# Kernel tuning notes

Hardware: AMD Instinct MI355X
Metric: run time of the kernel (lower is better)

## Reference

```python
import jax, jax.numpy as jnp
import numpy as np

N_NODES = 50000
N_EDGES = 800000
IN_DIM = 128
HID_DIM = 128
NUM_GRAPHS = 64


def gcn_conv(x, edge_index, W, b):
    """PyG GCNConv: symmetric-normalized aggregation with self-loops.
    out = D^{-1/2} (A + I) D^{-1/2} (x @ W) + b
    """
    n = x.shape[0]
    loop = jnp.arange(n, dtype=edge_index.dtype)
    src = jnp.concatenate([edge_index[0], loop])  # [E+N]
    dst = jnp.concatenate([edge_index[1], loop])
    deg = jax.ops.segment_sum(jnp.ones_like(dst, x.dtype), dst, num_segments=n)
    dinv = jnp.where(deg > 0, jax.lax.rsqrt(deg), 0.0)
    norm = dinv[src] * dinv[dst]  # [E+N]
    h = x @ W  # [N, H] transform before propagate (PyG order)
    msg = h[src] * norm[:, None]  # [E+N, H] gathered+scaled messages
    out = jax.ops.segment_sum(msg, dst, num_segments=n)  # scatter-add
    return out + b


def global_mean_pool(x, batch, num_graphs):
    s = jax.ops.segment_sum(x, batch, num_segments=num_graphs)
    cnt = jax.ops.segment_sum(jnp.ones((x.shape[0],), x.dtype), batch, num_segments=num_graphs)
    return s / jnp.maximum(cnt, 1.0)[:, None]


def setup_inputs() -> dict:
    key = jax.random.key(0)
    ks = jax.random.split(key, 8)
    x = jax.random.normal(ks[0], (N_NODES, IN_DIM), dtype=jnp.float32)
    edge_index = jax.random.randint(ks[1], (2, N_EDGES), 0, N_NODES, dtype=jnp.int64)
    batch = jnp.sort(jax.random.randint(ks[2], (N_NODES,), 0, NUM_GRAPHS, dtype=jnp.int64))
    s1 = 1.0 / np.sqrt(IN_DIM)
    s2 = 1.0 / np.sqrt(HID_DIM)
    W1 = jax.random.uniform(ks[3], (IN_DIM, HID_DIM), jnp.float32, -s1, s1)
    b1 = jnp.zeros((HID_DIM,), jnp.float32)
    W2 = jax.random.uniform(ks[4], (HID_DIM, HID_DIM), jnp.float32, -s2, s2)
    b2 = jnp.zeros((HID_DIM,), jnp.float32)
    Wc = jax.random.uniform(ks[5], (HID_DIM, 1), jnp.float32, -s2, s2)
    bc = jnp.zeros((1,), jnp.float32)
    return {"x": x, "edge_index": edge_index, "batch": batch,
            "W1": W1, "b1": b1, "W2": W2, "b2": b2, "Wc": Wc, "bc": bc}


def reference(x, edge_index, batch, W1, b1, W2, b2, Wc, bc):
    h = jax.nn.relu(gcn_conv(x, edge_index, W1, b1))
    # dropout p=0.1 is identity in eval mode
    h = gcn_conv(h, edge_index, W2, b2)
    g = global_mean_pool(h, batch, NUM_GRAPHS)  # [G, H]
    return jax.nn.sigmoid(g @ Wc + bc)  # [G, 1]
```

## Files before the change

### kernel.cpp

```cpp
#include <hip/hip_runtime.h>
#include <hip/hip_bf16.h>
#include <hip/hip_fp16.h>

#define N_NODES 50000
#define N_EDGES 800000
#define DIM     128
#define NG      64
#define GN      16
#define CAP     48
#define AGG_EB  256
#define LAXP    136

#define NBIN    196
#define SORT_B  250
#define EPB     3200

#define CAST_B  1563
#define VB_B    129
#define WF_B    8

typedef float  f2_t  __attribute__((ext_vector_type(2)));
typedef float  f32x4 __attribute__((ext_vector_type(4)));
typedef _Float16 f16x8 __attribute__((ext_vector_type(8)));
typedef _Float16 f16x4 __attribute__((ext_vector_type(4)));

__global__ void k_prep(const int* __restrict__ ei, int* __restrict__ binCnt,
                       const float4* __restrict__ x4, uint4* __restrict__ xq4,
                       const float* __restrict__ W2, const float* __restrict__ Wc,
                       const float* __restrict__ b2, float* __restrict__ v,
                       float* __restrict__ beta2,
                       const float* __restrict__ W1, f16x8* __restrict__ w1f) {
    __shared__ float red[4];
    __shared__ int hist[256];
    int bid = blockIdx.x, t = threadIdx.x;
    if (bid < SORT_B) {
        hist[t] = 0;
        __syncthreads();
        int base = bid * EPB;
        for (int r = 0; r < 13; r++) {
            int idx = r * 256 + t;
            if (idx < EPB) {
                int d = ei[N_EDGES + base + idx];
                atomicAdd(&hist[d >> 8], 1);
            }
        }
        __syncthreads();
        if (t < NBIN && hist[t] > 0) atomicAdd(&binCnt[t], hist[t]);
    } else if (bid < SORT_B + CAST_B) {
        int idx = (bid - SORT_B) * 256 + t;
        if (idx < N_NODES * DIM / 16) {
            uint4 o;
            unsigned* op = (unsigned*)&o;
            #pragma unroll
            for (int q = 0; q < 4; q++) {
                float4 f = x4[idx * 4 + q];
                int p = 0;
                p = __builtin_amdgcn_cvt_pk_fp8_f32(f.x, f.y, p, false);
                p = __builtin_amdgcn_cvt_pk_fp8_f32(f.z, f.w, p, true);
                op[q] = (unsigned)p;
            }
            xq4[idx] = o;
        }
    } else if (bid < SORT_B + CAST_B + VB_B) {
        int b = bid - (SORT_B + CAST_B);
        float p = 0.f;
        if (t < DIM) p = (b < DIM) ? W2[b * DIM + t] * Wc[t] : b2[t] * Wc[t];
        #pragma unroll
        for (int off = 32; off > 0; off >>= 1) p += __shfl_down(p, off, 64);
        if ((t & 63) == 0) red[t >> 6] = p;
        __syncthreads();
        if (t == 0) {
            float s = red[0] + red[1];
            if (b < DIM) v[b] = s; else beta2[0] = s;
        }
    } else {
        int idx = (bid - (SORT_B + CAST_B + VB_B)) * 256 + t;
        int ntile = idx >> 8, kb = (idx >> 6) & 3, l = idx & 63;
        int kbase = kb * 32 + (l >> 4) * 8;
        int n = ntile * 16 + (l & 15);
        f16x8 o;
        #pragma unroll
        for (int j = 0; j < 8; j++) o[j] = (_Float16)W1[(kbase + j) * DIM + n];
        w1f[idx] = o;
    }
}

__global__ void k_scatter(const int* __restrict__ ei, const int* __restrict__ binCnt,
                          int* __restrict__ binCur, int* __restrict__ binOff,
                          unsigned int* __restrict__ sorted) {
    __shared__ int soff[256];
    __shared__ int hist[256];
    __shared__ int cur[256];
    int bid = blockIdx.x, t = threadIdx.x;
    int c = (t < NBIN) ? binCnt[t] : 0;
    soff[t] = c;
    #pragma unroll
    for (int o = 1; o < 256; o <<= 1) {
        __syncthreads();
        int v2 = (t >= o) ? soff[t - o] : 0;
        __syncthreads();
        soff[t] += v2;
    }
    __syncthreads();
    int excl = soff[t] - c;
    if (bid == 0 && t < NBIN) binOff[t] = excl;
    hist[t] = 0;
    __syncthreads();
    int base = bid * EPB;
    for (int r = 0; r < 13; r++) {
        int idx = r * 256 + t;
        if (idx < EPB) {
            int d = ei[N_EDGES + base + idx];
            atomicAdd(&hist[d >> 8], 1);
        }
    }
    __syncthreads();
    if (t < NBIN && hist[t] > 0) cur[t] = excl + atomicAdd(&binCur[t], hist[t]);
    __syncthreads();
    for (int r = 0; r < 13; r++) {
        int idx = r * 256 + t;
        if (idx < EPB) {
            int e = base + idx;
            int s = ei[e];
            int d = ei[N_EDGES + e];
            int pos = atomicAdd(&cur[d >> 8], 1);
            sorted[pos] = (unsigned)s | ((unsigned)(d & 255) << 16);
        }
    }
}

__global__ void k_deg(const unsigned int* __restrict__ sorted,
                      const int* __restrict__ binOff, int* __restrict__ deg) {
    __shared__ int cnt[256];
    int b = blockIdx.x, t = threadIdx.x;
    cnt[t] = 0;
    __syncthreads();
    int lo = binOff[b];
    int hi = (b == NBIN - 1) ? N_EDGES : binOff[b + 1];
    for (int i = lo + t; i < hi; i += 256)
        atomicAdd(&cnt[sorted[i] >> 16], 1);
    __syncthreads();
    int node = b * 256 + t;
    if (node < N_NODES) deg[node] = cnt[t];
}

__global__ void k_build(const unsigned int* __restrict__ sorted,
                        const int* __restrict__ binOff, const int* __restrict__ deg,
                        unsigned int* __restrict__ csr) {
    __shared__ int cur[256];
    int b = blockIdx.x, t = threadIdx.x;
    cur[t] = 0;
    __syncthreads();
    int lo = binOff[b];
    int hi = (b == NBIN - 1) ? N_EDGES : binOff[b + 1];
    for (int i = lo + t; i < hi; i += 256) {
        unsigned e = sorted[i];
        unsigned src = e & 0xFFFFu;
        unsigned dLow = e >> 16;
        int pos = atomicAdd(&cur[dLow], 1);
        if (pos < CAP) {
            float w = rsqrtf((float)deg[src] + 1.f);
            unsigned hw = (unsigned)__half_as_ushort(__float2half(w));
            csr[(b * 256 + dLow) * CAP + pos] = src | (hw << 16);
        }
    }
}

__global__ __launch_bounds__(512) void k_node(
    const unsigned int* __restrict__ xq,
    const unsigned int* __restrict__ csr,
    const f16x8* __restrict__ w1f,
    const float* __restrict__ b1,
    const float* __restrict__ v, const int* __restrict__ deg,
    float* __restrict__ z2) {
    __shared__ _Float16 laxh[GN * LAXP];
    __shared__ float redm[GN * 8];
    int tid = threadIdx.x;
    int w = tid >> 6, l = tid & 63;
    int half = l >> 5, hl = l & 31;
    int node0 = blockIdx.x * GN;

    {
        int i = node0 + 2 * w + half;
        int len = min(deg[i], CAP);
        float di = rsqrtf((float)deg[i] + 1.f);

        unsigned su = xq[(size_t)i * 32 + hl];
        f2_t s01 = __builtin_amdgcn_cvt_pk_f32_fp8((int)su, false);
        f2_t s23 = __builtin_amdgcn_cvt_pk_f32_fp8((int)su, true);
        float ax[8], ay[8], az[8], aw[8];
        #pragma unroll
        for (int k = 0; k < 8; k++) { ax[k] = 0.f; ay[k] = 0.f; az[k] = 0.f; aw[k] = 0.f; }
        ax[0] = di * s01.x; ay[0] = di * s01.y;
        az[0] = di * s23.x; aw[0] = di * s23.y;

        int lenmax = max(len, __shfl_xor(len, 32, 64));
        int lmp = (lenmax + 7) & ~7;
        const uint4* csr4 = (const uint4*)csr;
        int base4 = i * (CAP / 4);
        for (int j = 0; j < lmp; j += 8) {
            uint4 ca = csr4[base4 + (j >> 2)];
            uint4 cb = csr4[base4 + (j >> 2) + 1];
            unsigned pe[8] = {ca.x, ca.y, ca.z, ca.w, cb.x, cb.y, cb.z, cb.w};
            unsigned q[8];
            #pragma unroll
            for (int k = 0; k < 8; k++)
                q[k] = xq[(size_t)(pe[k] & 0xFFFFu) * 32 + hl];
            float wgt[8];
            #pragma unroll
            for (int k = 0; k < 8; k++)
                wgt[k] = (j + k < len)
                    ? __half2float(__ushort_as_half((unsigned short)(pe[k] >> 16))) : 0.f;
            #pragma unroll
            for (int k = 0; k < 8; k++) {
                f2_t e01 = __builtin_amdgcn_cvt_pk_f32_fp8((int)q[k], false);
                f2_t e23 = __builtin_amdgcn_cvt_pk_f32_fp8((int)q[k], true);
                ax[k] = fmaf(wgt[k], e01.x, ax[k]);
                ay[k] = fmaf(wgt[k], e01.y, ay[k]);
                az[k] = fmaf(wgt[k], e23.x, az[k]);
                aw[k] = fmaf(wgt[k], e23.y, aw[k]);
            }
        }
        float a0 = 0.f, a1 = 0.f, a2 = 0.f, a3 = 0.f;
        #pragma unroll
        for (int k = 0; k < 8; k++) { a0 += ax[k]; a1 += ay[k]; a2 += az[k]; a3 += aw[k]; }
        f16x4 pk;
        pk[0] = (_Float16)(di * a0); pk[1] = (_Float16)(di * a1);
        pk[2] = (_Float16)(di * a2); pk[3] = (_Float16)(di * a3);
        *(f16x4*)&laxh[(2 * w + half) * LAXP + 4 * hl] = pk;
    }
    __syncthreads();

    f32x4 acc = {0.f, 0.f, 0.f, 0.f};
    #pragma unroll
    for (int kb = 0; kb < 4; kb++) {
        f16x8 af = *(const f16x8*)&laxh[(l & 15) * LAXP + kb * 32 + (l >> 4) * 8];
        f16x8 bf = w1f[(w * 4 + kb) * 64 + l];
        acc = __builtin_amdgcn_mfma_f32_16x16x32_f16(af, bf, acc, 0, 0, 0);
    }
    int n = w * 16 + (l & 15);
    float bn = b1[n], vn = v[n];
    #pragma unroll
    for (int r = 0; r < 4; r++) {
        float p = fmaxf(acc[r] + bn, 0.f) * vn;
        p += __shfl_xor(p, 1, 64);
        p += __shfl_xor(p, 2, 64);
        p += __shfl_xor(p, 4, 64);
        p += __shfl_xor(p, 8, 64);
        if ((l & 15) == 0) redm[((l >> 4) * 4 + r) * 8 + w] = p;
    }
    __syncthreads();
    if (tid < GN) {
        float s = 0.f;
        #pragma unroll
        for (int q = 0; q < 8; q++) s += redm[tid * 8 + q];
        z2[node0 + tid] = rsqrtf((float)deg[node0 + tid] + 1.f) * s;
    }
}

__global__ void k_aggz(const float* __restrict__ z2, const int* __restrict__ deg,
                       const int* __restrict__ ei, const int* __restrict__ batch,
                       float* __restrict__ gpartE, float* __restrict__ gpartN,
                       int* __restrict__ gcnt) {
    int bid = blockIdx.x, t = threadIdx.x;
    if (bid < AGG_EB) {
        __shared__ float bs[4][NG];
        bs[t >> 6][t & 63] = 0.f;
        __syncthreads();
        int wg = t >> 6;
        for (int base = bid * 1024; base < N_EDGES; base += AGG_EB * 1024) {
            #pragma unroll
            for (int k = 0; k < 4; k++) {
                int e = base + k * 256 + t;
                if (e < N_EDGES) {
                    int s = ei[e];
                    int d = ei[N_EDGES + e];
                    float dv = rsqrtf((float)deg[d] + 1.f);
                    atomicAdd(&bs[wg][batch[d]], dv * z2[s]);
                }
            }
        }
        __syncthreads();
        if (t < NG) gpartE[bid * NG + t] = bs[0][t] + bs[1][t] + bs[2][t] + bs[3][t];
    } else {
        __shared__ int range[2];
        __shared__ float rs[4];
        int g = bid - AGG_EB;
        if (t < 2) {
            int key = g + t;
            int lo = 0, hi = N_NODES;
            while (lo < hi) { int m = (lo + hi) >> 1; if (batch[m] < key) lo = m + 1; else hi = m; }
            range[t] = lo;
        }
        __syncthreads();
        int lo = range[0], hi = range[1];
        float loc = 0.f;
        for (int i = lo + t; i < hi; i += 256)
            loc += rsqrtf((float)deg[i] + 1.f) * z2[i];
        #pragma unroll
        for (int off = 32; off > 0; off >>= 1) loc += __shfl_down(loc, off, 64);
        if ((t & 63) == 0) rs[t >> 6] = loc;
        __syncthreads();
        if (t == 0) {
            gpartN[g] = rs[0] + rs[1] + rs[2] + rs[3];
            gcnt[g] = hi - lo;
        }
    }
}

__global__ void k_final(const float* __restrict__ gpartE, const float* __restrict__ gpartN,
                        const int* __restrict__ gcnt, const float* __restrict__ beta2,
                        const float* __restrict__ bcin, float* __restrict__ out) {
    __shared__ float acc[4][NG];
    int t = threadIdx.x;
    int g = t & 63, c = t >> 6;
    float s = 0.f;
    for (int k = 0; k < AGG_EB / 4; k++)
        s += gpartE[(c * (AGG_EB / 4) + k) * NG + g];
    acc[c][g] = s;
    __syncthreads();
    if (t < NG) {
        float tot = acc[0][t] + acc[1][t] + acc[2][t] + acc[3][t] + gpartN[t];
        int cnt = gcnt[t];
        float val = tot / (float)(cnt > 0 ? cnt : 1) + beta2[0] + bcin[0];
        out[t] = 1.f / (1.f + expf(-val));
    }
}

extern "C" void kernel_launch(void* const* d_in, const int* in_sizes, int n_in,
                              void* d_out, int out_size, void* d_ws, size_t ws_size,
                              hipStream_t stream) {
    const float* x   = (const float*)d_in[0];
    const int*   ei  = (const int*)  d_in[1];
    const int*   bat = (const int*)  d_in[2];
    const float* W1  = (const float*)d_in[3];
    const float* b1  = (const float*)d_in[4];
    const float* W2  = (const float*)d_in[5];
    const float* b2  = (const float*)d_in[6];
    const float* Wc  = (const float*)d_in[7];
    const float* bc  = (const float*)d_in[8];
    float* out = (float*)d_out;

    char* w = (char*)d_ws;
    size_t off = 0;
    auto alloc = [&](size_t bytes) -> void* {
        void* p = w + off;
        off = (off + bytes + 255) & ~(size_t)255;
        return p;
    };
    int*   binCnt  = (int*)  alloc(NBIN * 4);
    int*   binCur  = (int*)  alloc(NBIN * 4);
    size_t zero_len = off;
    int*   binOff  = (int*)  alloc(NBIN * 4);
    int*   deg     = (int*)  alloc(N_NODES * 4);
    float* z2      = (float*)alloc(N_NODES * 4);
    float* v       = (float*)alloc(DIM * 4);
    float* beta2   = (float*)alloc(4);
    float* gpartE  = (float*)alloc((size_t)AGG_EB * NG * 4);
    float* gpartN  = (float*)alloc(NG * 4);
    int*   gcnt    = (int*)  alloc(NG * 4);
    f16x8* w1f     = (f16x8*)alloc(2048 * 16);
    unsigned int* xq     = (unsigned int*)alloc((size_t)N_NODES * DIM);
    unsigned int* sorted = (unsigned int*)alloc((size_t)N_EDGES * 4);
    unsigned int* csr    = (unsigned int*)alloc((size_t)N_NODES * CAP * 4);
    (void)ws_size; (void)in_sizes; (void)n_in; (void)out_size;

    hipMemsetAsync(d_ws, 0, zero_len, stream);

    dim3 b256(256);
    k_prep<<<dim3(SORT_B + CAST_B + VB_B + WF_B), b256, 0, stream>>>(
        ei, binCnt, (const float4*)x, (uint4*)xq, W2, Wc, b2, v, beta2, W1, w1f);
    k_scatter<<<dim3(SORT_B), b256, 0, stream>>>(ei, binCnt, binCur, binOff, sorted);
    k_deg<<<dim3(NBIN), b256, 0, stream>>>(sorted, binOff, deg);
    k_build<<<dim3(NBIN), b256, 0, stream>>>(sorted, binOff, deg, csr);
    k_node<<<dim3(N_NODES / GN), dim3(512), 0, stream>>>(
        xq, csr, w1f, b1, v, deg, z2);
    k_aggz<<<dim3(AGG_EB + NG), b256, 0, stream>>>(z2, deg, ei, bat, gpartE, gpartN, gcnt);
    k_final<<<dim3(1), b256, 0, stream>>>(gpartE, gpartN, gcnt, beta2, bc, out);
}
```

Baseline: 169.9 us.

## Build CSR with global atomics and prescale features by source degree

Replaces the binned counting sort (histogram, scatter, deg, build kernels) with a single pass that uses global atomicAdd on per-node degree to place 16-bit source ids directly into a fixed-capacity CSR. The source-side normalization is folded into the fp8 feature cast (x scaled by dinv before quantization), so the aggregation loop becomes plain adds with a zero sentinel row for padding. It also packs batch id and fp16 dinv per node for the pooling kernel. This removes three launches and the sorted buffer and halves CSR size, but the neighbor order within each CSR row is now nondeterministic and it relies on heavy global atomic contention.

```diff
diff --git a/kernel.cpp b/kernel.cpp
--- a/kernel.cpp
+++ b/kernel.cpp
@@ -11,10 +11,7 @@
 #define AGG_EB  256
 #define LAXP    136
 
-#define NBIN    196
-#define SORT_B  250
-#define EPB     3200
-
+#define BUILD_B 782
 #define CAST_B  1563
 #define VB_B    129
 #define WF_B    8
@@ -24,45 +21,28 @@
 typedef _Float16 f16x8 __attribute__((ext_vector_type(8)));
 typedef _Float16 f16x4 __attribute__((ext_vector_type(4)));
 
-__global__ void k_prep(const int* __restrict__ ei, int* __restrict__ binCnt,
-                       const float4* __restrict__ x4, uint4* __restrict__ xq4,
+__global__ void k_prep(const int* __restrict__ ei, int* __restrict__ deg,
+                       unsigned short* __restrict__ csr,
                        const float* __restrict__ W2, const float* __restrict__ Wc,
                        const float* __restrict__ b2, float* __restrict__ v,
                        float* __restrict__ beta2,
                        const float* __restrict__ W1, f16x8* __restrict__ w1f) {
     __shared__ float red[4];
-    __shared__ int hist[256];
     int bid = blockIdx.x, t = threadIdx.x;
-    if (bid < SORT_B) {
-        hist[t] = 0;
-        __syncthreads();
-        int base = bid * EPB;
-        for (int r = 0; r < 13; r++) {
-            int idx = r * 256 + t;
-            if (idx < EPB) {
-                int d = ei[N_EDGES + base + idx];
-                atomicAdd(&hist[d >> 8], 1);
-            }
-        }
-        __syncthreads();
-        if (t < NBIN && hist[t] > 0) atomicAdd(&binCnt[t], hist[t]);
-    } else if (bid < SORT_B + CAST_B) {
-        int idx = (bid - SORT_B) * 256 + t;
-        if (idx < N_NODES * DIM / 16) {
-            uint4 o;
-            unsigned* op = (unsigned*)&o;
-            #pragma unroll
-            for (int q = 0; q < 4; q++) {
-                float4 f = x4[idx * 4 + q];
-                int p = 0;
-                p = __builtin_amdgcn_cvt_pk_fp8_f32(f.x, f.y, p, false);
-                p = __builtin_amdgcn_cvt_pk_fp8_f32(f.z, f.w, p, true);
-                op[q] = (unsigned)p;
-            }
-            xq4[idx] = o;
-        }
-    } else if (bid < SORT_B + CAST_B + VB_B) {
-        int b = bid - (SORT_B + CAST_B);
+    if (bid < BUILD_B) {
+        int base = bid * 1024;
+        #pragma unroll
+        for (int k = 0; k < 4; k++) {
+            int e = base + k * 256 + t;
+            if (e < N_EDGES) {
+                int s = ei[e];
+                int d = ei[N_EDGES + e];
+                int pos = atomicAdd(&deg[d], 1);
+                if (pos < CAP) csr[(size_t)d * CAP + pos] = (unsigned short)s;
+            }
+        }
+    } else if (bid < BUILD_B + VB_B) {
+        int b = bid - BUILD_B;
         float p = 0.f;
         if (t < DIM) p = (b < DIM) ? W2[b * DIM + t] * Wc[t] : b2[t] * Wc[t];
         #pragma unroll
@@ -74,7 +54,7 @@
             if (b < DIM) v[b] = s; else beta2[0] = s;
         }
     } else {
-        int idx = (bid - (SORT_B + CAST_B + VB_B)) * 256 + t;
+        int idx = (bid - (BUILD_B + VB_B)) * 256 + t;
         int ntile = idx >> 8, kb = (idx >> 6) & 3, l = idx & 63;
         int kbase = kb * 32 + (l >> 4) * 8;
         int n = ntile * 16 + (l & 15);
@@ -85,90 +65,37 @@
     }
 }
 
-__global__ void k_scatter(const int* __restrict__ ei, const int* __restrict__ binCnt,
-                          int* __restrict__ binCur, int* __restrict__ binOff,
-                          unsigned int* __restrict__ sorted) {
-    __shared__ int soff[256];
-    __shared__ int hist[256];
-    __shared__ int cur[256];
-    int bid = blockIdx.x, t = threadIdx.x;
-    int c = (t < NBIN) ? binCnt[t] : 0;
-    soff[t] = c;
+__global__ void k_cast(const float4* __restrict__ x4, uint4* __restrict__ xq4,
+                       const int* __restrict__ deg, const int* __restrict__ batch,
+                       unsigned int* __restrict__ bd) {
+    int idx = blockIdx.x * 256 + threadIdx.x;
+    if (idx >= (N_NODES + 1) * 8) return;
+    if (idx >= N_NODES * 8) {
+        xq4[idx] = make_uint4(0u, 0u, 0u, 0u);
+        return;
+    }
+    int node = idx >> 3;
+    float di = rsqrtf((float)deg[node] + 1.f);
+    uint4 o;
+    unsigned* op = (unsigned*)&o;
     #pragma unroll
-    for (int o = 1; o < 256; o <<= 1) {
-        __syncthreads();
-        int v2 = (t >= o) ? soff[t - o] : 0;
-        __syncthreads();
-        soff[t] += v2;
-    }
-    __syncthreads();
-    int excl = soff[t] - c;
-    if (bid == 0 && t < NBIN) binOff[t] = excl;
-    hist[t] = 0;
-    __syncthreads();
-    int base = bid * EPB;
-    for (int r = 0; r < 13; r++) {
-        int idx = r * 256 + t;
-        if (idx < EPB) {
-            int d = ei[N_EDGES + base + idx];
-            atomicAdd(&hist[d >> 8], 1);
-        }
-    }
-    __syncthreads();
-    if (t < NBIN && hist[t] > 0) cur[t] = excl + atomicAdd(&binCur[t], hist[t]);
-    __syncthreads();
-    for (int r = 0; r < 13; r++) {
-        int idx = r * 256 + t;
-        if (idx < EPB) {
-            int e = base + idx;
-            int s = ei[e];
-            int d = ei[N_EDGES + e];
-            int pos = atomicAdd(&cur[d >> 8], 1);
-            sorted[pos] = (unsigned)s | ((unsigned)(d & 255) << 16);
-        }
-    }
-}
-
-__global__ void k_deg(const unsigned int* __restrict__ sorted,
-                      const int* __restrict__ binOff, int* __restrict__ deg) {
-    __shared__ int cnt[256];
-    int b = blockIdx.x, t = threadIdx.x;
-    cnt[t] = 0;
-    __syncthreads();
-    int lo = binOff[b];
-    int hi = (b == NBIN - 1) ? N_EDGES : binOff[b + 1];
-    for (int i = lo + t; i < hi; i += 256)
-        atomicAdd(&cnt[sorted[i] >> 16], 1);
-    __syncthreads();
-    int node = b * 256 + t;
-    if (node < N_NODES) deg[node] = cnt[t];
-}
-
-__global__ void k_build(const unsigned int* __restrict__ sorted,
-                        const int* __restrict__ binOff, const int* __restrict__ deg,
-                        unsigned int* __restrict__ csr) {
-    __shared__ int cur[256];
-    int b = blockIdx.x, t = threadIdx.x;
-    cur[t] = 0;
-    __syncthreads();
-    int lo = binOff[b];
-    int hi = (b == NBIN - 1) ? N_EDGES : binOff[b + 1];
-    for (int i = lo + t; i < hi; i += 256) {
-        unsigned e = sorted[i];
-        unsigned src = e & 0xFFFFu;
-        unsigned dLow = e >> 16;
-        int pos = atomicAdd(&cur[dLow], 1);
-        if (pos < CAP) {
-            float w = rsqrtf((float)deg[src] + 1.f);
-            unsigned hw = (unsigned)__half_as_ushort(__float2half(w));
-            csr[(b * 256 + dLow) * CAP + pos] = src | (hw << 16);
-        }
+    for (int q = 0; q < 4; q++) {
+        float4 f = x4[idx * 4 + q];
+        int p = 0;
+        p = __builtin_amdgcn_cvt_pk_fp8_f32(di * f.x, di * f.y, p, false);
+        p = __builtin_amdgcn_cvt_pk_fp8_f32(di * f.z, di * f.w, p, true);
+        op[q] = (unsigned)p;
+    }
+    xq4[idx] = o;
+    if ((idx & 7) == 0) {
+        unsigned hw = (unsigned)__half_as_ushort(__float2half(di));
+        bd[node] = ((unsigned)batch[node] & 0xFFFFu) | (hw << 16);
     }
 }
 
 __global__ __launch_bounds__(512) void k_node(
     const unsigned int* __restrict__ xq,
-    const unsigned int* __restrict__ csr,
+    const unsigned short* __restrict__ csr,
     const f16x8* __restrict__ w1f,
     const float* __restrict__ b1,
     const float* __restrict__ v, const int* __restrict__ deg,
@@ -182,8 +109,9 @@
 
     {
         int i = node0 + 2 * w + half;
-        int len = min(deg[i], CAP);
-        float di = rsqrtf((float)deg[i] + 1.f);
+        int dg = deg[i];
+        int len = min(dg, CAP);
+        float di = rsqrtf((float)dg + 1.f);
 
         unsigned su = xq[(size_t)i * 32 + hl];
         f2_t s01 = __builtin_amdgcn_cvt_pk_f32_fp8((int)su, false);
@@ -191,34 +119,28 @@
         float ax[8], ay[8], az[8], aw[8];
         #pragma unroll
         for (int k = 0; k < 8; k++) { ax[k] = 0.f; ay[k] = 0.f; az[k] = 0.f; aw[k] = 0.f; }
-        ax[0] = di * s01.x; ay[0] = di * s01.y;
-        az[0] = di * s23.x; aw[0] = di * s23.y;
+        ax[0] = s01.x; ay[0] = s01.y;
+        az[0] = s23.x; aw[0] = s23.y;
 
         int lenmax = max(len, __shfl_xor(len, 32, 64));
         int lmp = (lenmax + 7) & ~7;
-        const uint4* csr4 = (const uint4*)csr;
-        int base4 = i * (CAP / 4);
+        const uint4* csr4 = (const uint4*)(csr + (size_t)i * CAP);
         for (int j = 0; j < lmp; j += 8) {
-            uint4 ca = csr4[base4 + (j >> 2)];
-            uint4 cb = csr4[base4 + (j >> 2) + 1];
-            unsigned pe[8] = {ca.x, ca.y, ca.z, ca.w, cb.x, cb.y, cb.z, cb.w};
+            uint4 cw = csr4[j >> 3];
+            unsigned cw8[4] = {cw.x, cw.y, cw.z, cw.w};
             unsigned q[8];
             #pragma unroll
-            for (int k = 0; k < 8; k++)
-                q[k] = xq[(size_t)(pe[k] & 0xFFFFu) * 32 + hl];
-            float wgt[8];
-            #pragma unroll
-            for (int k = 0; k < 8; k++)
-                wgt[k] = (j + k < len)
-                    ? __half2float(__ushort_as_half((unsigned short)(pe[k] >> 16))) : 0.f;
+            for (int k = 0; k < 8; k++) {
+                unsigned id = (cw8[k >> 1] >> ((k & 1) * 16)) & 0xFFFFu;
+                unsigned idc = (j + k < len) ? id : (unsigned)N_NODES;
+                q[k] = xq[(size_t)idc * 32 + hl];
+            }
             #pragma unroll
             for (int k = 0; k < 8; k++) {
                 f2_t e01 = __builtin_amdgcn_cvt_pk_f32_fp8((int)q[k], false);
                 f2_t e23 = __builtin_amdgcn_cvt_pk_f32_fp8((int)q[k], true);
-                ax[k] = fmaf(wgt[k], e01.x, ax[k]);
-                ay[k] = fmaf(wgt[k], e01.y, ay[k]);
-                az[k] = fmaf(wgt[k], e23.x, az[k]);
-                aw[k] = fmaf(wgt[k], e23.y, aw[k]);
+                ax[k] += e01.x; ay[k] += e01.y;
+                az[k] += e23.x; aw[k] += e23.y;
             }
         }
         float a0 = 0.f, a1 = 0.f, a2 = 0.f, a3 = 0.f;
@@ -258,7 +180,7 @@
     }
 }
 
-__global__ void k_aggz(const float* __restrict__ z2, const int* __restrict__ deg,
+__global__ void k_aggz(const float* __restrict__ z2, const unsigned int* __restrict__ bd,
                        const int* __restrict__ ei, const int* __restrict__ batch,
                        float* __restrict__ gpartE, float* __restrict__ gpartN,
                        int* __restrict__ gcnt) {
@@ -275,8 +197,9 @@
                 if (e < N_EDGES) {
                     int s = ei[e];
                     int d = ei[N_EDGES + e];
-                    float dv = rsqrtf((float)deg[d] + 1.f);
-                    atomicAdd(&bs[wg][batch[d]], dv * z2[s]);
+                    unsigned u = bd[d];
+                    float dv = __half2float(__ushort_as_half((unsigned short)(u >> 16)));
+                    atomicAdd(&bs[wg][u & 63u], dv * z2[s]);
                 }
             }
         }
@@ -296,7 +219,7 @@
         int lo = range[0], hi = range[1];
         float loc = 0.f;
         for (int i = lo + t; i < hi; i += 256)
-            loc += rsqrtf((float)deg[i] + 1.f) * z2[i];
+            loc += __half2float(__ushort_as_half((unsigned short)(bd[i] >> 16))) * z2[i];
         #pragma unroll
         for (int off = 32; off > 0; off >>= 1) loc += __shfl_down(loc, off, 64);
         if ((t & 63) == 0) rs[t >> 6] = loc;
@@ -348,33 +271,29 @@
         off = (off + bytes + 255) & ~(size_t)255;
         return p;
     };
-    int*   binCnt  = (int*)  alloc(NBIN * 4);
-    int*   binCur  = (int*)  alloc(NBIN * 4);
+    int*   deg     = (int*)  alloc(N_NODES * 4);
     size_t zero_len = off;
-    int*   binOff  = (int*)  alloc(NBIN * 4);
-    int*   deg     = (int*)  alloc(N_NODES * 4);
     float* z2      = (float*)alloc(N_NODES * 4);
     float* v       = (float*)alloc(DIM * 4);
     float* beta2   = (float*)alloc(4);
     float* gpartE  = (float*)alloc((size_t)AGG_EB * NG * 4);
     float* gpartN  = (float*)alloc(NG * 4);
     int*   gcnt    = (int*)  alloc(NG * 4);
+    unsigned int* bd = (unsigned int*)alloc(N_NODES * 4);
     f16x8* w1f     = (f16x8*)alloc(2048 * 16);
-    unsigned int* xq     = (unsigned int*)alloc((size_t)N_NODES * DIM);
-    unsigned int* sorted = (unsigned int*)alloc((size_t)N_EDGES * 4);
-    unsigned int* csr    = (unsigned int*)alloc((size_t)N_NODES * CAP * 4);
+    unsigned int* xq = (unsigned int*)alloc((size_t)(N_NODES + 1) * DIM);
+    unsigned short* csr = (unsigned short*)alloc((size_t)N_NODES * CAP * 2);
     (void)ws_size; (void)in_sizes; (void)n_in; (void)out_size;
 
     hipMemsetAsync(d_ws, 0, zero_len, stream);
 
     dim3 b256(256);
-    k_prep<<<dim3(SORT_B + CAST_B + VB_B + WF_B), b256, 0, stream>>>(
-        ei, binCnt, (const float4*)x, (uint4*)xq, W2, Wc, b2, v, beta2, W1, w1f);
-    k_scatter<<<dim3(SORT_B), b256, 0, stream>>>(ei, binCnt, binCur, binOff, sorted);
-    k_deg<<<dim3(NBIN), b256, 0, stream>>>(sorted, binOff, deg);
-    k_build<<<dim3(NBIN), b256, 0, stream>>>(sorted, binOff, deg, csr);
+    k_prep<<<dim3(BUILD_B + VB_B + WF_B), b256, 0, stream>>>(
+        ei, deg, csr, W2, Wc, b2, v, beta2, W1, w1f);
+    k_cast<<<dim3(CAST_B), b256, 0, stream>>>(
+        (const float4*)x, (uint4*)xq, deg, bat, bd);
     k_node<<<dim3(N_NODES / GN), dim3(512), 0, stream>>>(
         xq, csr, w1f, b1, v, deg, z2);
-    k_aggz<<<dim3(AGG_EB + NG), b256, 0, stream>>>(z2, deg, ei, bat, gpartE, gpartN, gcnt);
+    k_aggz<<<dim3(AGG_EB + NG), b256, 0, stream>>>(z2, bd, ei, bat, gpartE, gpartN, gcnt);
     k_final<<<dim3(1), b256, 0, stream>>>(gpartE, gpartN, gcnt, beta2, bc, out);
 }
```

Result: slower. 193.3 us (+13.8%).
